# Kernel optimization log

Measured on AMD Instinct MI355X. Metric: run time of the kernel, lower is better.

## Reference

```python
import jax, jax.numpy as jnp
import numpy as np

BS, RAL, LAL = 128, 1024, 256
CS, VOC, HFS, EMB = 256, 34, 512, 256


def setup_inputs() -> dict:
    key0 = jax.random.key(0)
    ks = jax.random.split(key0, 16)
    s = 0.02
    # mask from random valid lengths (at least 1 valid frame per example)
    lengths = jax.random.randint(ks[15], (BS,), RAL // 2, RAL + 1)
    mask = (jnp.arange(RAL)[None, :] < lengths[:, None]).astype(jnp.float32)
    return {
        "key": jax.random.normal(ks[0], (BS, RAL, CS), jnp.float32),
        "val": jax.random.normal(ks[1], (BS, RAL, CS), jnp.float32),
        "mask": mask,
        "emb": jax.random.normal(ks[2], (VOC, EMB), jnp.float32) * s,
        "Wih_a": jax.random.normal(ks[3], (4 * HFS, EMB + CS), jnp.float32) * s,
        "Whh_a": jax.random.normal(ks[4], (4 * HFS, HFS), jnp.float32) * s,
        "bih_a": jnp.zeros((4 * HFS,), jnp.float32),
        "bhh_a": jnp.zeros((4 * HFS,), jnp.float32),
        "Wih_b": jax.random.normal(ks[5], (4 * HFS, HFS), jnp.float32) * s,
        "Whh_b": jax.random.normal(ks[6], (4 * HFS, HFS), jnp.float32) * s,
        "bih_b": jnp.zeros((4 * HFS,), jnp.float32),
        "bhh_b": jnp.zeros((4 * HFS,), jnp.float32),
        "Wq": jax.random.normal(ks[7], (CS, HFS), jnp.float32) * s,
        "bq": jnp.zeros((CS,), jnp.float32),
        "Wc": jax.random.normal(ks[8], (VOC, HFS + CS), jnp.float32) * s,
        "bc": jnp.zeros((VOC,), jnp.float32),
        "y": jax.random.randint(ks[9], (BS, LAL), 0, VOC, jnp.int32),
    }


def _lstm_cell(x, h, c, Wih, Whh, bih, bhh):
    z = x @ Wih.T + bih + h @ Whh.T + bhh  # (BS, 4H)
    i, f, g, o = jnp.split(z, 4, axis=-1)
    i, f, o = jax.nn.sigmoid(i), jax.nn.sigmoid(f), jax.nn.sigmoid(o)
    g = jnp.tanh(g)
    c2 = f * c + i * g
    return o * jnp.tanh(c2), c2


def _attend(key, val, query, mask):
    # energy: (BS, RAL) = bmm(key, query[...,None])
    energy = jnp.einsum("brc,bc->br", key, query)
    att = jax.nn.softmax(energy, axis=1) * mask
    att = att / jnp.sum(att, axis=1, keepdims=True)
    return jnp.einsum("br,brc->bc", att, val)  # context (BS, CS)


def reference(key, val, mask, emb, Wih_a, Whh_a, bih_a, bhh_a,
              Wih_b, Whh_b, bih_b, bhh_b, Wq, bq, Wc, bc, y):
    bs = y.shape[0]
    z = jnp.zeros((bs, HFS), jnp.float32)
    init = (z, z, z, z, jnp.zeros((bs, CS), jnp.float32))

    def step(carry, y_t):
        ha, ca, hb, cb, ctx = carry
        e = emb[y_t]  # (BS, EMB)
        x = jnp.concatenate([e, ctx], axis=1)
        ha, ca = _lstm_cell(x, ha, ca, Wih_a, Whh_a, bih_a, bhh_a)
        hb, cb = _lstm_cell(ha, hb, cb, Wih_b, Whh_b, bih_b, bhh_b)
        query = hb @ Wq.T + bq  # (BS, CS)
        ctx = _attend(key, val, query, mask)
        logits = jnp.concatenate([hb, ctx], axis=1) @ Wc.T + bc  # (BS, VOC)
        return (ha, ca, hb, cb, ctx), logits

    _, preds = jax.lax.scan(step, init, y.T)  # (LAL, BS, VOC)
    return jnp.transpose(preds, (1, 0, 2))  # (BS, LAL, VOC)
```

## Files before the change

### kernel.cpp

```cpp
#include <hip/hip_runtime.h>
#include <cstdint>
#include <cstddef>

static constexpr int BS  = 128;
static constexpr int RAL = 1024;
static constexpr int LAL = 256;
static constexpr int CS  = 256;
static constexpr int VOC = 34;
static constexpr int HFS = 512;
static constexpr int EMB = 256;

typedef float  f32x4  __attribute__((ext_vector_type(4)));
typedef short  bf16x8 __attribute__((ext_vector_type(8)));

static __device__ __forceinline__ float bflo(unsigned int u) {
    return __builtin_bit_cast(float, u << 16);
}
static __device__ __forceinline__ float bfhi(unsigned int u) {
    return __builtin_bit_cast(float, u & 0xffff0000u);
}
static __device__ __forceinline__ unsigned short f2bf(float f) {
    unsigned int x = __builtin_bit_cast(unsigned int, f);
    x = (x + 0x7fffu + ((x >> 16) & 1u)) >> 16;
    return (unsigned short)x;
}
static __device__ __forceinline__ float sigf(float x)   { return 1.0f / (1.0f + __expf(-x)); }
static __device__ __forceinline__ float tanhf_(float x) { return 1.0f - 2.0f / (__expf(2.0f * x) + 1.0f); }

__global__ void cvt4_kernel(const float4* __restrict__ in, ushort4* __restrict__ out, int n4) {
    int i  = blockIdx.x * blockDim.x + threadIdx.x;
    int st = gridDim.x * blockDim.x;
    for (; i < n4; i += st) {
        float4 v = in[i];
        ushort4 o;
        o.x = f2bf(v.x); o.y = f2bf(v.y); o.z = f2bf(v.z); o.w = f2bf(v.w);
        out[i] = o;
    }
}

__global__ __launch_bounds__(256) void len_kernel(const float* __restrict__ mask, int* __restrict__ Llen) {
    __shared__ int red[256];
    const int b = blockIdx.x, tid = threadIdx.x;
    int c = 0;
    for (int r = tid; r < RAL; r += 256) c += (mask[b * RAL + r] != 0.0f) ? 1 : 0;
    red[tid] = c;
    __syncthreads();
    for (int s = 128; s > 0; s >>= 1) {
        if (tid < s) red[tid] += red[tid + s];
        __syncthreads();
    }
    if (tid == 0) Llen[b] = red[0];
}

__global__ __launch_bounds__(256) void lstm_kernel(
    const unsigned short* __restrict__ p0, int s0,
    const unsigned short* __restrict__ p1, int s1,
    const unsigned short* __restrict__ p2, int s2,
    const unsigned short* __restrict__ p3, int s3,
    const int* __restrict__ yidx, int t,
    const unsigned short* __restrict__ Wih, const unsigned short* __restrict__ Whh,
    const float* __restrict__ bih, const float* __restrict__ bhh,
    float* __restrict__ cst,
    unsigned short* __restrict__ hout)
{
    __shared__ __align__(16) float zp[3][4][64][4];

    const int tid  = threadIdx.x;
    const int lane = tid & 63;
    const int wv   = tid >> 6;
    const int quad = lane >> 4;
    const int l16  = lane & 15;
    const int j    = blockIdx.x * 16 + l16;
    const int mrow = blockIdx.y * 16 + l16;

    const unsigned short* pa;
    const unsigned short* wb;
    {
        const unsigned short* const ps[4] = {p0, p1, p2, p3};
        const int ss[4] = {s0, s1, s2, s3};
        long rbase;
        if (wv == 0 && yidx) rbase = (long)yidx[mrow * LAL + t] * ss[0];
        else                 rbase = (long)mrow * ss[wv];
        pa = ps[wv] + rbase + quad * 8;
        const unsigned short* Wp = (wv < 2) ? Wih : Whh;
        wb = Wp + (wv & 1) * 256 + quad * 8;
    }

    const unsigned short* wg[4];
#pragma unroll
    for (int g = 0; g < 4; ++g) wg[g] = wb + (long)(g * HFS + j) * HFS;

    f32x4 acc[4];
#pragma unroll
    for (int g = 0; g < 4; ++g) acc[g] = (f32x4)0.0f;

#pragma unroll
    for (int kc = 0; kc < 8; ++kc) {
        bf16x8 a  = *(const bf16x8*)(pa + kc * 32);
        bf16x8 b0 = *(const bf16x8*)(wg[0] + kc * 32);
        bf16x8 b1 = *(const bf16x8*)(wg[1] + kc * 32);
        bf16x8 b2 = *(const bf16x8*)(wg[2] + kc * 32);
        bf16x8 b3 = *(const bf16x8*)(wg[3] + kc * 32);
        acc[0] = __builtin_amdgcn_mfma_f32_16x16x32_bf16(a, b0, acc[0], 0, 0, 0);
        acc[1] = __builtin_amdgcn_mfma_f32_16x16x32_bf16(a, b1, acc[1], 0, 0, 0);
        acc[2] = __builtin_amdgcn_mfma_f32_16x16x32_bf16(a, b2, acc[2], 0, 0, 0);
        acc[3] = __builtin_amdgcn_mfma_f32_16x16x32_bf16(a, b3, acc[3], 0, 0, 0);
    }

    if (wv != 0) {
#pragma unroll
        for (int g = 0; g < 4; ++g)
            *(f32x4*)&zp[wv - 1][g][lane][0] = acc[g];
    }
    __syncthreads();
    if (wv == 0) {
#pragma unroll
        for (int g = 0; g < 4; ++g) {
            acc[g] += *(const f32x4*)&zp[0][g][lane][0];
            acc[g] += *(const f32x4*)&zp[1][g][lane][0];
            acc[g] += *(const f32x4*)&zp[2][g][lane][0];
        }
        const float bI = bih[j]           + bhh[j];
        const float bF = bih[HFS + j]     + bhh[HFS + j];
        const float bG = bih[2 * HFS + j] + bhh[2 * HFS + j];
        const float bO = bih[3 * HFS + j] + bhh[3 * HFS + j];
#pragma unroll
        for (int r = 0; r < 4; ++r) {
            int m   = blockIdx.y * 16 + quad * 4 + r;
            int idx = m * HFS + j;
            float iv = sigf(acc[0][r] + bI);
            float fv = sigf(acc[1][r] + bF);
            float gv = tanhf_(acc[2][r] + bG);
            float ov = sigf(acc[3][r] + bO);
            float cn = fv * cst[idx] + iv * gv;
            cst[idx] = cn;
            hout[idx] = f2bf(ov * tanhf_(cn));
        }
    }
}

template <bool KVBF>
__global__ __launch_bounds__(1024) void attn_kernel(
    const void* __restrict__ keyp, const void* __restrict__ valp,
    const int* __restrict__ Llen,
    const unsigned short* __restrict__ hbv,
    const unsigned short* __restrict__ Wqb,
    const float* __restrict__ bq,
    const float* __restrict__ Wc, const float* __restrict__ bc,
    unsigned short* __restrict__ ctxbf,
    float* __restrict__ outp, int t)
{
    __shared__ __align__(16) float xcat[HFS + CS];
    __shared__ __align__(16) float q_lds[CS];
    __shared__ __align__(16) float e_lds[RAL];
    __shared__ __align__(16) float ctxp[16][CS];
    __shared__ float red[32];

    const int tid = threadIdx.x;
    const int b   = blockIdx.x;
    const int L   = Llen[b];

    if (tid < HFS) xcat[tid] = bflo((unsigned int)hbv[b * HFS + tid]);
    __syncthreads();

    {
        const int c  = tid >> 2;
        const int jj = tid & 3;
        const unsigned short* wr = Wqb + (long)c * HFS + jj * 128;
        const float* xr = &xcat[jj * 128];
        float qa = 0.0f;
#pragma unroll
        for (int k = 0; k < 128; k += 8) {
            uint4 u = *(const uint4*)(wr + k);
            float4 h0 = *(const float4*)(xr + k);
            float4 h1 = *(const float4*)(xr + k + 4);
            qa += bflo(u.x) * h0.x + bfhi(u.x) * h0.y
                + bflo(u.y) * h0.z + bfhi(u.y) * h0.w
                + bflo(u.z) * h1.x + bfhi(u.z) * h1.y
                + bflo(u.w) * h1.z + bfhi(u.w) * h1.w;
        }
        qa += __shfl_xor(qa, 1);
        qa += __shfl_xor(qa, 2);
        if (jj == 0) q_lds[c] = qa + bq[c];
    }
    __syncthreads();

    {
        const int jj   = tid & 7;
        const int rloc = tid >> 3;
        for (int r0 = 0; r0 < L; r0 += 128) {
            const int r = r0 + rloc;
            float acc = 0.0f;
            if (r < L) {
                if (KVBF) {
                    const unsigned short* kp = (const unsigned short*)keyp + ((long)b * RAL + r) * CS + jj * 32;
#pragma unroll
                    for (int i = 0; i < 4; ++i) {
                        uint4 u = *(const uint4*)(kp + i * 8);
                        const float* qp = &q_lds[jj * 32 + i * 8];
                        float4 qa  = *(const float4*)qp;
                        float4 qb2 = *(const float4*)(qp + 4);
                        acc += bflo(u.x) * qa.x  + bfhi(u.x) * qa.y
                             + bflo(u.y) * qa.z  + bfhi(u.y) * qa.w
                             + bflo(u.z) * qb2.x + bfhi(u.z) * qb2.y
                             + bflo(u.w) * qb2.z + bfhi(u.w) * qb2.w;
                    }
                } else {
                    const float* kp = (const float*)keyp + ((long)b * RAL + r) * CS + jj * 32;
#pragma unroll
                    for (int i = 0; i < 8; ++i) {
                        float4 kv = *(const float4*)(kp + i * 4);
                        float4 qa = *(const float4*)&q_lds[jj * 32 + i * 4];
                        acc += kv.x * qa.x + kv.y * qa.y + kv.z * qa.z + kv.w * qa.w;
                    }
                }
            }
            acc += __shfl_xor(acc, 1);
            acc += __shfl_xor(acc, 2);
            acc += __shfl_xor(acc, 4);
            if (jj == 0 && r < L) e_lds[r] = acc;
        }
    }
    __syncthreads();

    float pm = (tid < L) ? e_lds[tid] : -1e30f;
#pragma unroll
    for (int s = 32; s > 0; s >>= 1) pm = fmaxf(pm, __shfl_xor(pm, s));
    if ((tid & 63) == 0) red[tid >> 6] = pm;
    __syncthreads();
    float M = red[0];
#pragma unroll
    for (int i = 1; i < 16; ++i) M = fmaxf(M, red[i]);

    float ps = 0.0f;
    if (tid < L) { float v = __expf(e_lds[tid] - M); e_lds[tid] = v; ps = v; }
#pragma unroll
    for (int s = 32; s > 0; s >>= 1) ps += __shfl_xor(ps, s);
    if ((tid & 63) == 0) red[16 + (tid >> 6)] = ps;
    __syncthreads();
    float S = 0.0f;
#pragma unroll
    for (int i = 0; i < 16; ++i) S += red[16 + i];
    const float invS = 1.0f / S;

    {
        const int wv = tid >> 6;
        const int c4 = (tid & 63) * 4;
        float a0 = 0.f, a1 = 0.f, a2 = 0.f, a3 = 0.f;
        if (KVBF) {
            const unsigned short* vb = (const unsigned short*)valp + (long)b * RAL * CS + c4;
            int r = wv;
            for (; r + 48 < L; r += 64) {
                uint2 u0 = *(const uint2*)(vb + (long)(r)      * CS);
                uint2 u1 = *(const uint2*)(vb + (long)(r + 16) * CS);
                uint2 u2 = *(const uint2*)(vb + (long)(r + 32) * CS);
                uint2 u3 = *(const uint2*)(vb + (long)(r + 48) * CS);
                float w0 = e_lds[r], w1 = e_lds[r + 16], w2 = e_lds[r + 32], w3 = e_lds[r + 48];
                a0 += w0 * bflo(u0.x) + w1 * bflo(u1.x) + w2 * bflo(u2.x) + w3 * bflo(u3.x);
                a1 += w0 * bfhi(u0.x) + w1 * bfhi(u1.x) + w2 * bfhi(u2.x) + w3 * bfhi(u3.x);
                a2 += w0 * bflo(u0.y) + w1 * bflo(u1.y) + w2 * bflo(u2.y) + w3 * bflo(u3.y);
                a3 += w0 * bfhi(u0.y) + w1 * bfhi(u1.y) + w2 * bfhi(u2.y) + w3 * bfhi(u3.y);
            }
            for (; r < L; r += 16) {
                uint2 u = *(const uint2*)(vb + (long)r * CS);
                float w = e_lds[r];
                a0 += w * bflo(u.x); a1 += w * bfhi(u.x);
                a2 += w * bflo(u.y); a3 += w * bfhi(u.y);
            }
        } else {
            const float* vb = (const float*)valp + (long)b * RAL * CS + c4;
            int r = wv;
            for (; r + 48 < L; r += 64) {
                float4 v0 = *(const float4*)(vb + (long)(r)      * CS);
                float4 v1 = *(const float4*)(vb + (long)(r + 16) * CS);
                float4 v2 = *(const float4*)(vb + (long)(r + 32) * CS);
                float4 v3 = *(const float4*)(vb + (long)(r + 48) * CS);
                float w0 = e_lds[r], w1 = e_lds[r + 16], w2 = e_lds[r + 32], w3 = e_lds[r + 48];
                a0 += w0 * v0.x + w1 * v1.x + w2 * v2.x + w3 * v3.x;
                a1 += w0 * v0.y + w1 * v1.y + w2 * v2.y + w3 * v3.y;
                a2 += w0 * v0.z + w1 * v1.z + w2 * v2.z + w3 * v3.z;
                a3 += w0 * v0.w + w1 * v1.w + w2 * v2.w + w3 * v3.w;
            }
            for (; r < L; r += 16) {
                float4 v = *(const float4*)(vb + (long)r * CS);
                float w = e_lds[r];
                a0 += w * v.x; a1 += w * v.y; a2 += w * v.z; a3 += w * v.w;
            }
        }
        float4 out4 = {a0, a1, a2, a3};
        *(float4*)&ctxp[tid >> 6][c4] = out4;
    }
    __syncthreads();

    if (tid < CS) {
        float cv = 0.0f;
#pragma unroll
        for (int w = 0; w < 16; ++w) cv += ctxp[w][tid];
        cv *= invS;
        xcat[HFS + tid] = cv;
        ctxbf[b * CS + tid] = f2bf(cv);
    }
    __syncthreads();

    if (tid < VOC * 8) {
        const int v   = tid >> 3;
        const int jj2 = tid & 7;
        const float* wr = Wc + (long)v * (HFS + CS) + jj2 * 96;
        const float* xr = &xcat[jj2 * 96];
        float part = 0.0f;
#pragma unroll
        for (int i = 0; i < 24; ++i) {
            float4 wv4 = *(const float4*)(wr + i * 4);
            float4 xv  = *(const float4*)(xr + i * 4);
            part += wv4.x * xv.x + wv4.y * xv.y + wv4.z * xv.z + wv4.w * xv.w;
        }
        part += __shfl_xor(part, 1);
        part += __shfl_xor(part, 2);
        part += __shfl_xor(part, 4);
        if (jj2 == 0)
            outp[((long)b * LAL + t) * VOC + v] = part + bc[v];
    }
}

extern "C" void kernel_launch(void* const* d_in, const int* in_sizes, int n_in,
                              void* d_out, int out_size, void* d_ws, size_t ws_size,
                              hipStream_t stream)
{
    (void)in_sizes; (void)n_in; (void)out_size;
    const float* keyf  = (const float*)d_in[0];
    const float* valf  = (const float*)d_in[1];
    const float* mask  = (const float*)d_in[2];
    const float* embf  = (const float*)d_in[3];
    const float* WihAf = (const float*)d_in[4];
    const float* WhhAf = (const float*)d_in[5];
    const float* bihA  = (const float*)d_in[6];
    const float* bhhA  = (const float*)d_in[7];
    const float* WihBf = (const float*)d_in[8];
    const float* WhhBf = (const float*)d_in[9];
    const float* bihB  = (const float*)d_in[10];
    const float* bhhB  = (const float*)d_in[11];
    const float* Wqf   = (const float*)d_in[12];
    const float* bq    = (const float*)d_in[13];
    const float* Wc    = (const float*)d_in[14];
    const float* bc    = (const float*)d_in[15];
    const int*   y     = (const int*)d_in[16];
    float* outp = (float*)d_out;

    size_t off = 0;
    auto take = [&](size_t bytes) -> void* {
        void* p = (char*)d_ws + off;
        off += (bytes + 255) & ~(size_t)255;
        return p;
    };

    unsigned short* ha    = (unsigned short*)take((size_t)2 * BS * HFS * 2);
    unsigned short* hbuf  = (unsigned short*)take((size_t)2 * BS * HFS * 2);
    float*          ca    = (float*)take((size_t)BS * HFS * 4);
    float*          cbuf  = (float*)take((size_t)BS * HFS * 4);
    unsigned short* ctxbf = (unsigned short*)take((size_t)BS * CS * 2);
    size_t stateBytes = off;

    int*            Llen  = (int*)take((size_t)BS * 4);
    unsigned short* embb  = (unsigned short*)take((size_t)VOC * EMB * 2);
    unsigned short* WihAb = (unsigned short*)take((size_t)4 * HFS * HFS * 2);
    unsigned short* WhhAb = (unsigned short*)take((size_t)4 * HFS * HFS * 2);
    unsigned short* WihBb = (unsigned short*)take((size_t)4 * HFS * HFS * 2);
    unsigned short* WhhBb = (unsigned short*)take((size_t)4 * HFS * HFS * 2);
    unsigned short* Wqb   = (unsigned short*)take((size_t)CS * HFS * 2);

    const size_t kvBytes = (size_t)BS * RAL * CS * 2;
    unsigned short* keyb = nullptr;
    unsigned short* valb = nullptr;
    bool kvbf = false;
    bool keyInVal = false;
    if (off + 2 * (kvBytes + 256) <= ws_size) {
        keyb = (unsigned short*)take(kvBytes);
        valb = (unsigned short*)take(kvBytes);
        kvbf = true;
    } else if (off + kvBytes + 256 <= ws_size) {
        valb = (unsigned short*)take(kvBytes);
        keyb = (unsigned short*)d_in[1];
        kvbf = true;
        keyInVal = true;
    }

    hipMemsetAsync(d_ws, 0, stateBytes, stream);
    len_kernel<<<dim3(BS), dim3(256), 0, stream>>>(mask, Llen);

    auto cvt = [&](const float* src, unsigned short* dst, long n) {
        int n4 = (int)(n / 4);
        int blocks = (n4 + 255) / 256;
        if (blocks > 8192) blocks = 8192;
        cvt4_kernel<<<dim3(blocks), dim3(256), 0, stream>>>((const float4*)src, (ushort4*)dst, n4);
    };
    cvt(embf,  embb,  (long)VOC * EMB);
    cvt(WihAf, WihAb, (long)4 * HFS * HFS);
    cvt(WhhAf, WhhAb, (long)4 * HFS * HFS);
    cvt(WihBf, WihBb, (long)4 * HFS * HFS);
    cvt(WhhBf, WhhBb, (long)4 * HFS * HFS);
    cvt(Wqf,   Wqb,   (long)CS * HFS);
    if (kvbf) {
        if (keyInVal) {
            cvt(valf, valb, (long)BS * RAL * CS);
            cvt(keyf, keyb, (long)BS * RAL * CS);
        } else {
            cvt(keyf, keyb, (long)BS * RAL * CS);
            cvt(valf, valb, (long)BS * RAL * CS);
        }
    }

    for (int t = 0; t < LAL; ++t) {
        unsigned short* haIn  = ha   + (t & 1) * (BS * HFS);
        unsigned short* haOut = ha   + ((t + 1) & 1) * (BS * HFS);
        unsigned short* hbIn  = hbuf + (t & 1) * (BS * HFS);
        unsigned short* hbOut = hbuf + ((t + 1) & 1) * (BS * HFS);

        lstm_kernel<<<dim3(32, 8), dim3(256), 0, stream>>>(
            embb, EMB, ctxbf, CS, haIn, HFS, haIn + 256, HFS,
            y, t, WihAb, WhhAb, bihA, bhhA, ca, haOut);

        lstm_kernel<<<dim3(32, 8), dim3(256), 0, stream>>>(
            haOut, HFS, haOut + 256, HFS, hbIn, HFS, hbIn + 256, HFS,
            nullptr, t, WihBb, WhhBb, bihB, bhhB, cbuf, hbOut);

        if (kvbf)
            attn_kernel<true><<<dim3(BS), dim3(1024), 0, stream>>>(
                keyb, valb, Llen, hbOut, Wqb, bq, Wc, bc, ctxbf, outp, t);
        else
            attn_kernel<false><<<dim3(BS), dim3(1024), 0, stream>>>(
                keyf, valf, Llen, hbOut, Wqb, bq, Wc, bc, ctxbf, outp, t);
    }
}
```

Baseline: 12.97 ms.

## Transpose value tensor to bf16 column-major and use bf16 dot2 instructions in attention

Adds a preprocessing kernel that stores the value tensor transposed as bf16, so each thread reduces one context channel over contiguous rows and the cross-wave context reduction and one barrier go away. Query, key-score and context dot products switch to packed bf16 dot2 instructions, with the query and softmax weights kept in bf16 in shared memory. The transposed reduction now reads all rows regardless of the valid length, adding memory traffic for padded frames and extra rounding of the attention weights.

```diff
diff --git a/kernel.cpp b/kernel.cpp
--- a/kernel.cpp
+++ b/kernel.cpp
@@ -26,6 +26,18 @@
 }
 static __device__ __forceinline__ float sigf(float x)   { return 1.0f / (1.0f + __expf(-x)); }
 static __device__ __forceinline__ float tanhf_(float x) { return 1.0f - 2.0f / (__expf(2.0f * x) + 1.0f); }
+
+#if __has_builtin(__builtin_amdgcn_fdot2_f32_bf16)
+typedef __bf16 bf16x2v __attribute__((ext_vector_type(2)));
+static __device__ __forceinline__ float dot2bf(unsigned int a, unsigned int b, float c) {
+    return __builtin_amdgcn_fdot2_f32_bf16(__builtin_bit_cast(bf16x2v, a),
+                                           __builtin_bit_cast(bf16x2v, b), c, false);
+}
+#else
+static __device__ __forceinline__ float dot2bf(unsigned int a, unsigned int b, float c) {
+    return c + bflo(a) * bflo(b) + bfhi(a) * bfhi(b);
+}
+#endif
 
 __global__ void cvt4_kernel(const float4* __restrict__ in, ushort4* __restrict__ out, int n4) {
     int i  = blockIdx.x * blockDim.x + threadIdx.x;
@@ -35,6 +47,43 @@
         ushort4 o;
         o.x = f2bf(v.x); o.y = f2bf(v.y); o.z = f2bf(v.z); o.w = f2bf(v.w);
         out[i] = o;
+    }
+}
+
+__global__ __launch_bounds__(256) void transpose_val(const float* __restrict__ val,
+                                                     unsigned short* __restrict__ VT) {
+    __shared__ float tile[64][68];
+    const int b  = blockIdx.y;
+    const int rt = blockIdx.x >> 2;
+    const int ct = blockIdx.x & 3;
+    const int t  = threadIdx.x;
+
+    const float* src = val + (long)b * RAL * CS + (long)(rt * 64) * CS + ct * 64;
+    {
+        const int rl = t >> 4;
+        const int c4 = (t & 15) * 4;
+#pragma unroll
+        for (int j = 0; j < 4; ++j) {
+            int rr = rl + j * 16;
+            float4 v = *(const float4*)(src + (long)rr * CS + c4);
+            *(float4*)&tile[rr][c4] = v;
+        }
+    }
+    __syncthreads();
+    {
+        const int cl   = t >> 2;
+        const int rseg = t & 3;
+        unsigned short* dst = VT + (long)b * RAL * CS + (long)(ct * 64 + cl) * RAL + rt * 64;
+#pragma unroll
+        for (int s = 0; s < 4; ++s) {
+            int r0 = rseg * 16 + s * 4;
+            ushort4 o;
+            o.x = f2bf(tile[r0 + 0][cl]);
+            o.y = f2bf(tile[r0 + 1][cl]);
+            o.z = f2bf(tile[r0 + 2][cl]);
+            o.w = f2bf(tile[r0 + 3][cl]);
+            *(ushort4*)(dst + r0) = o;
+        }
     }
 }
 
@@ -139,7 +188,7 @@
     }
 }
 
-template <bool KVBF>
+template <int TIER>
 __global__ __launch_bounds__(1024) void attn_kernel(
     const void* __restrict__ keyp, const void* __restrict__ valp,
     const int* __restrict__ Llen,
@@ -151,8 +200,11 @@
     float* __restrict__ outp, int t)
 {
     __shared__ __align__(16) float xcat[HFS + CS];
+    __shared__ __align__(16) unsigned short hb_bf[HFS];
+    __shared__ __align__(16) unsigned short q_bf[CS];
     __shared__ __align__(16) float q_lds[CS];
     __shared__ __align__(16) float e_lds[RAL];
+    __shared__ __align__(16) unsigned short ew[RAL];
     __shared__ __align__(16) float ctxp[16][CS];
     __shared__ float red[32];
 
@@ -160,28 +212,49 @@
     const int b   = blockIdx.x;
     const int L   = Llen[b];
 
-    if (tid < HFS) xcat[tid] = bflo((unsigned int)hbv[b * HFS + tid]);
+    if (tid < HFS) {
+        unsigned short h = hbv[b * HFS + tid];
+        hb_bf[tid] = h;
+        xcat[tid]  = bflo((unsigned int)h);
+    }
     __syncthreads();
 
     {
         const int c  = tid >> 2;
         const int jj = tid & 3;
         const unsigned short* wr = Wqb + (long)c * HFS + jj * 128;
-        const float* xr = &xcat[jj * 128];
         float qa = 0.0f;
-#pragma unroll
-        for (int k = 0; k < 128; k += 8) {
-            uint4 u = *(const uint4*)(wr + k);
-            float4 h0 = *(const float4*)(xr + k);
-            float4 h1 = *(const float4*)(xr + k + 4);
-            qa += bflo(u.x) * h0.x + bfhi(u.x) * h0.y
-                + bflo(u.y) * h0.z + bfhi(u.y) * h0.w
-                + bflo(u.z) * h1.x + bfhi(u.z) * h1.y
-                + bflo(u.w) * h1.z + bfhi(u.w) * h1.w;
+        if (TIER == 2) {
+            const unsigned short* hr = &hb_bf[jj * 128];
+#pragma unroll
+            for (int k = 0; k < 128; k += 8) {
+                uint4 wu = *(const uint4*)(wr + k);
+                uint4 hu = *(const uint4*)(hr + k);
+                qa = dot2bf(wu.x, hu.x, qa);
+                qa = dot2bf(wu.y, hu.y, qa);
+                qa = dot2bf(wu.z, hu.z, qa);
+                qa = dot2bf(wu.w, hu.w, qa);
+            }
+        } else {
+            const float* xr = &xcat[jj * 128];
+#pragma unroll
+            for (int k = 0; k < 128; k += 8) {
+                uint4 u = *(const uint4*)(wr + k);
+                float4 h0 = *(const float4*)(xr + k);
+                float4 h1 = *(const float4*)(xr + k + 4);
+                qa += bflo(u.x) * h0.x + bfhi(u.x) * h0.y
+                    + bflo(u.y) * h0.z + bfhi(u.y) * h0.w
+                    + bflo(u.z) * h1.x + bfhi(u.z) * h1.y
+                    + bflo(u.w) * h1.z + bfhi(u.w) * h1.w;
+            }
         }
         qa += __shfl_xor(qa, 1);
         qa += __shfl_xor(qa, 2);
-        if (jj == 0) q_lds[c] = qa + bq[c];
+        if (jj == 0) {
+            float qv = qa + bq[c];
+            if (TIER == 2) q_bf[c] = f2bf(qv);
+            else           q_lds[c] = qv;
+        }
     }
     __syncthreads();
 
@@ -190,21 +263,21 @@
         const int rloc = tid >> 3;
         for (int r0 = 0; r0 < L; r0 += 128) {
             const int r = r0 + rloc;
-            float acc = 0.0f;
+            float acc = 0.0f, acc1 = 0.0f;
             if (r < L) {
-                if (KVBF) {
+                if (TIER == 2) {
                     const unsigned short* kp = (const unsigned short*)keyp + ((long)b * RAL + r) * CS + jj * 32;
+                    const unsigned short* qp = &q_bf[jj * 32];
 #pragma unroll
                     for (int i = 0; i < 4; ++i) {
-                        uint4 u = *(const uint4*)(kp + i * 8);
-                        const float* qp = &q_lds[jj * 32 + i * 8];
-                        float4 qa  = *(const float4*)qp;
-                        float4 qb2 = *(const float4*)(qp + 4);
-                        acc += bflo(u.x) * qa.x  + bfhi(u.x) * qa.y
-                             + bflo(u.y) * qa.z  + bfhi(u.y) * qa.w
-                             + bflo(u.z) * qb2.x + bfhi(u.z) * qb2.y
-                             + bflo(u.w) * qb2.z + bfhi(u.w) * qb2.w;
+                        uint4 ku = *(const uint4*)(kp + i * 8);
+                        uint4 qu = *(const uint4*)(qp + i * 8);
+                        acc  = dot2bf(ku.x, qu.x, acc);
+                        acc1 = dot2bf(ku.y, qu.y, acc1);
+                        acc  = dot2bf(ku.z, qu.z, acc);
+                        acc1 = dot2bf(ku.w, qu.w, acc1);
                     }
+                    acc += acc1;
                 } else {
                     const float* kp = (const float*)keyp + ((long)b * RAL + r) * CS + jj * 32;
 #pragma unroll
@@ -233,7 +306,14 @@
     for (int i = 1; i < 16; ++i) M = fmaxf(M, red[i]);
 
     float ps = 0.0f;
-    if (tid < L) { float v = __expf(e_lds[tid] - M); e_lds[tid] = v; ps = v; }
+    if (tid < L) {
+        float v = __expf(e_lds[tid] - M);
+        e_lds[tid] = v;
+        ew[tid] = f2bf(v);
+        ps = v;
+    } else {
+        ew[tid] = 0;
+    }
 #pragma unroll
     for (int s = 32; s > 0; s >>= 1) ps += __shfl_xor(ps, s);
     if ((tid & 63) == 0) red[16 + (tid >> 6)] = ps;
@@ -243,64 +323,67 @@
     for (int i = 0; i < 16; ++i) S += red[16 + i];
     const float invS = 1.0f / S;
 
-    {
+    if (TIER == 2) {
+        const int c  = tid >> 2;
+        const int jj = tid & 3;
+        const unsigned short* vtb = (const unsigned short*)valp + (long)b * RAL * CS + (long)c * RAL + jj * 256;
+        const unsigned short* wp  = &ew[jj * 256];
+        float a0 = 0.0f, a1 = 0.0f;
+#pragma unroll 4
+        for (int rr = 0; rr < 256; rr += 8) {
+            uint4 vu = *(const uint4*)(vtb + rr);
+            uint4 wu = *(const uint4*)(wp + rr);
+            a0 = dot2bf(vu.x, wu.x, a0);
+            a1 = dot2bf(vu.y, wu.y, a1);
+            a0 = dot2bf(vu.z, wu.z, a0);
+            a1 = dot2bf(vu.w, wu.w, a1);
+        }
+        float a = a0 + a1;
+        a += __shfl_xor(a, 1);
+        a += __shfl_xor(a, 2);
+        if (jj == 0) {
+            float cv = a * invS;
+            xcat[HFS + c] = cv;
+            ctxbf[b * CS + c] = f2bf(cv);
+        }
+    } else {
         const int wv = tid >> 6;
         const int c4 = (tid & 63) * 4;
         float a0 = 0.f, a1 = 0.f, a2 = 0.f, a3 = 0.f;
-        if (KVBF) {
-            const unsigned short* vb = (const unsigned short*)valp + (long)b * RAL * CS + c4;
-            int r = wv;
-            for (; r + 48 < L; r += 64) {
-                uint2 u0 = *(const uint2*)(vb + (long)(r)      * CS);
-                uint2 u1 = *(const uint2*)(vb + (long)(r + 16) * CS);
-                uint2 u2 = *(const uint2*)(vb + (long)(r + 32) * CS);
-                uint2 u3 = *(const uint2*)(vb + (long)(r + 48) * CS);
-                float w0 = e_lds[r], w1 = e_lds[r + 16], w2 = e_lds[r + 32], w3 = e_lds[r + 48];
-                a0 += w0 * bflo(u0.x) + w1 * bflo(u1.x) + w2 * bflo(u2.x) + w3 * bflo(u3.x);
-                a1 += w0 * bfhi(u0.x) + w1 * bfhi(u1.x) + w2 * bfhi(u2.x) + w3 * bfhi(u3.x);
-                a2 += w0 * bflo(u0.y) + w1 * bflo(u1.y) + w2 * bflo(u2.y) + w3 * bflo(u3.y);
-                a3 += w0 * bfhi(u0.y) + w1 * bfhi(u1.y) + w2 * bfhi(u2.y) + w3 * bfhi(u3.y);
-            }
-            for (; r < L; r += 16) {
-                uint2 u = *(const uint2*)(vb + (long)r * CS);
-                float w = e_lds[r];
-                a0 += w * bflo(u.x); a1 += w * bfhi(u.x);
-                a2 += w * bflo(u.y); a3 += w * bfhi(u.y);
-            }
-        } else {
-            const float* vb = (const float*)valp + (long)b * RAL * CS + c4;
-            int r = wv;
-            for (; r + 48 < L; r += 64) {
-                float4 v0 = *(const float4*)(vb + (long)(r)      * CS);
-                float4 v1 = *(const float4*)(vb + (long)(r + 16) * CS);
-                float4 v2 = *(const float4*)(vb + (long)(r + 32) * CS);
-                float4 v3 = *(const float4*)(vb + (long)(r + 48) * CS);
-                float w0 = e_lds[r], w1 = e_lds[r + 16], w2 = e_lds[r + 32], w3 = e_lds[r + 48];
-                a0 += w0 * v0.x + w1 * v1.x + w2 * v2.x + w3 * v3.x;
-                a1 += w0 * v0.y + w1 * v1.y + w2 * v2.y + w3 * v3.y;
-                a2 += w0 * v0.z + w1 * v1.z + w2 * v2.z + w3 * v3.z;
-                a3 += w0 * v0.w + w1 * v1.w + w2 * v2.w + w3 * v3.w;
-            }
-            for (; r < L; r += 16) {
-                float4 v = *(const float4*)(vb + (long)r * CS);
-                float w = e_lds[r];
-                a0 += w * v.x; a1 += w * v.y; a2 += w * v.z; a3 += w * v.w;
-            }
+        const float* vb = (const float*)valp + (long)b * RAL * CS + c4;
+        int r = wv;
+        for (; r + 48 < L; r += 64) {
+            float4 v0 = *(const float4*)(vb + (long)(r)      * CS);
+            float4 v1 = *(const float4*)(vb + (long)(r + 16) * CS);
+            float4 v2 = *(const float4*)(vb + (long)(r + 32) * CS);
+            float4 v3 = *(const float4*)(vb + (long)(r + 48) * CS);
+            float w0 = e_lds[r], w1 = e_lds[r + 16], w2 = e_lds[r + 32], w3 = e_lds[r + 48];
+            a0 += w0 * v0.x + w1 * v1.x + w2 * v2.x + w3 * v3.x;
+            a1 += w0 * v0.y + w1 * v1.y + w2 * v2.y + w3 * v3.y;
+            a2 += w0 * v0.z + w1 * v1.z + w2 * v2.z + w3 * v3.z;
+            a3 += w0 * v0.w + w1 * v1.w + w2 * v2.w + w3 * v3.w;
+        }
+        for (; r < L; r += 16) {
+            float4 v = *(const float4*)(vb + (long)r * CS);
+            float w = e_lds[r];
+            a0 += w * v.x; a1 += w * v.y; a2 += w * v.z; a3 += w * v.w;
         }
         float4 out4 = {a0, a1, a2, a3};
-        *(float4*)&ctxp[tid >> 6][c4] = out4;
-    }
-    __syncthreads();
-
-    if (tid < CS) {
-        float cv = 0.0f;
-#pragma unroll
-        for (int w = 0; w < 16; ++w) cv += ctxp[w][tid];
-        cv *= invS;
-        xcat[HFS + tid] = cv;
-        ctxbf[b * CS + tid] = f2bf(cv);
-    }
-    __syncthreads();
+        *(float4*)&ctxp[wv][c4] = out4;
+    }
+    __syncthreads();
+
+    if (TIER != 2) {
+        if (tid < CS) {
+            float cv = 0.0f;
+#pragma unroll
+            for (int w = 0; w < 16; ++w) cv += ctxp[w][tid];
+            cv *= invS;
+            xcat[HFS + tid] = cv;
+            ctxbf[b * CS + tid] = f2bf(cv);
+        }
+        __syncthreads();
+    }
 
     if (tid < VOC * 8) {
         const int v   = tid >> 3;
@@ -370,17 +453,17 @@
 
     const size_t kvBytes = (size_t)BS * RAL * CS * 2;
     unsigned short* keyb = nullptr;
-    unsigned short* valb = nullptr;
-    bool kvbf = false;
+    unsigned short* VT   = nullptr;
+    int tier = 0;
     bool keyInVal = false;
     if (off + 2 * (kvBytes + 256) <= ws_size) {
         keyb = (unsigned short*)take(kvBytes);
-        valb = (unsigned short*)take(kvBytes);
-        kvbf = true;
+        VT   = (unsigned short*)take(kvBytes);
+        tier = 2;
     } else if (off + kvBytes + 256 <= ws_size) {
-        valb = (unsigned short*)take(kvBytes);
+        VT   = (unsigned short*)take(kvBytes);
         keyb = (unsigned short*)d_in[1];
-        kvbf = true;
+        tier = 2;
         keyInVal = true;
     }
 
@@ -399,14 +482,10 @@
     cvt(WihBf, WihBb, (long)4 * HFS * HFS);
     cvt(WhhBf, WhhBb, (long)4 * HFS * HFS);
     cvt(Wqf,   Wqb,   (long)CS * HFS);
-    if (kvbf) {
-        if (keyInVal) {
-            cvt(valf, valb, (long)BS * RAL * CS);
-            cvt(keyf, keyb, (long)BS * RAL * CS);
-        } else {
-            cvt(keyf, keyb, (long)BS * RAL * CS);
-            cvt(valf, valb, (long)BS * RAL * CS);
-        }
+    if (tier == 2) {
+        transpose_val<<<dim3(64, BS), dim3(256), 0, stream>>>(valf, VT);
+        cvt(keyf, keyb, (long)BS * RAL * CS);
+        (void)keyInVal;
     }
 
     for (int t = 0; t < LAL; ++t) {
@@ -423,11 +502,11 @@
             haOut, HFS, haOut + 256, HFS, hbIn, HFS, hbIn + 256, HFS,
             nullptr, t, WihBb, WhhBb, bihB, bhhB, cbuf, hbOut);
 
-        if (kvbf)
-            attn_kernel<true><<<dim3(BS), dim3(1024), 0, stream>>>(
-                keyb, valb, Llen, hbOut, Wqb, bq, Wc, bc, ctxbf, outp, t);
+        if (tier == 2)
+            attn_kernel<2><<<dim3(BS), dim3(1024), 0, stream>>>(
+                keyb, VT, Llen, hbOut, Wqb, bq, Wc, bc, ctxbf, outp, t);
         else
-            attn_kernel<false><<<dim3(BS), dim3(1024), 0, stream>>>(
+            attn_kernel<0><<<dim3(BS), dim3(1024), 0, stream>>>(
                 keyf, valf, Llen, hbOut, Wqb, bq, Wc, bc, ctxbf, outp, t);
     }
 }
```

New measurement: 14.60 ms. +12.6%, slower.
